# Optimization experiments

Measured on AMD Instinct MI355X. Metric: run time of the kernel, lower is better.

The kernel has to match this reference:

```python
import jax, jax.numpy as jnp
import numpy as np

N, NN = 16384, 10          # n_messages, max neighbors
IN, H = 135, 256           # input feature size, hidden size
HEADS, DPH = 4, 256 // 4   # attention heads, dim per head
DEPTH = 5
NEG_INF = -1e18


def setup_inputs() -> dict:
    key = jax.random.key(0)
    ks = jax.random.split(key, 17)
    s = lambda k, sh: (jax.random.normal(k, sh, jnp.float32) * 0.05)
    return {
        "fmess": jax.random.normal(ks[0], (N, IN), jnp.float32),
        "bgraph": jax.random.randint(ks[1], (N, NN), 0, N),
        "Wq": s(ks[2], (H, IN)), "bq": s(ks[3], (H,)),
        "Wk": s(ks[4], (H, H)), "bk": s(ks[5], (H,)),
        "Wv": s(ks[6], (H, H)), "bv": s(ks[7], (H,)),
        "alpha": s(ks[8], (1, 1, HEADS, 2 * DPH)),
        "abias": s(ks[9], (1, 1, HEADS)),
        "Wz": s(ks[10], (H, IN + H)), "bz": s(ks[11], (H,)),
        "Wr": s(ks[12], (H, IN)),
        "Ur": s(ks[13], (H, H)), "bur": s(ks[14], (H,)),
        "Wh": s(ks[15], (H, IN + H)), "bh": s(ks[16], (H,)),
    }


def reference(fmess, bgraph, Wq, bq, Wk, bk, Wv, bv, alpha, abias,
              Wz, bz, Wr, Ur, bur, Wh, bh):
    n = fmess.shape[0]
    # q depends only on fmess -> compute once (identical math to per-step recompute)
    q = (fmess @ Wq.T + bq).reshape(n, 1, HEADS, DPH)
    node_mask = jnp.ones((n, 1), jnp.float32).at[0, 0].set(0.0)

    def step(h, _):
        h_nei = h[bgraph]                                   # [n, nn, H] gather
        k = (h_nei @ Wk.T + bk).reshape(n, NN, HEADS, DPH)
        v = (h_nei @ Wv.T + bv).reshape(n, NN, HEADS, DPH)
        qb = jnp.broadcast_to(q, (n, NN, HEADS, DPH))
        qk = jax.nn.leaky_relu(jnp.concatenate([qb, k], axis=-1))  # slope 0.01
        score = jnp.sum(qk * alpha, axis=-1) + abias        # [n, nn, heads]
        attn_mask = (jnp.sum(h_nei, axis=2) == 0)[:, :, None]
        score = jnp.where(attn_mask, NEG_INF, score)
        w = jax.nn.softmax(score, axis=1)                   # softmax over neighbors
        sum_h = jnp.einsum('nmh,nmhd->nhd', w, v).reshape(n, H)
        z = jax.nn.sigmoid(jnp.concatenate([fmess, sum_h], axis=1) @ Wz.T + bz)
        r = jax.nn.sigmoid(fmess @ Wr.T + sum_h @ Ur.T + bur)
        pre_h = jnp.tanh(jnp.concatenate([fmess, r * sum_h], axis=1) @ Wh.T + bh)
        new_h = ((1.0 - z) * sum_h + z * pre_h) * node_mask
        return new_h, None

    h0 = jnp.zeros((n, H), jnp.float32)
    h, _ = jax.lax.scan(step, h0, None, length=DEPTH)
    return h
```

## Files before the change

### kernel.cpp

```cpp
#include <hip/hip_runtime.h>
#include <hip/hip_bf16.h>
#include <math.h>

#define NMSG 16384
#define NNEI 10
#define INF_ 135
#define KPAD 160
#define HID 256
#define DPH 64
#define DEPTH 5

typedef __attribute__((ext_vector_type(8))) short short8b;
typedef __attribute__((ext_vector_type(4))) float f32x4;
typedef __hip_bfloat16 bf16;

__device__ __forceinline__ float sigmoidf_(float x){ return 1.f/(1.f+expf(-x)); }
__device__ __forceinline__ float b2f(unsigned short u){ return __uint_as_float(((unsigned)u)<<16); }

__device__ __forceinline__ void gload_lds16(const void* g, void* l){
    __builtin_amdgcn_global_load_lds(
        (const __attribute__((address_space(1))) unsigned int*)g,
        (__attribute__((address_space(3))) unsigned int*)l, 16, 0, 0);
}

template<int EPI>
__global__ __launch_bounds__(256) void mm_k(
    const bf16* __restrict__ A, const bf16* __restrict__ B, int K,
    float* __restrict__ Cf,
    bf16* __restrict__ Cb0, bf16* __restrict__ Cb1, bf16* __restrict__ Cb2,
    const bf16* __restrict__ E0, const bf16* __restrict__ E1,
    const float* __restrict__ b0, const float* __restrict__ b1,
    const bf16* __restrict__ SH, const bf16* __restrict__ ZBB,
    const float* __restrict__ AL, float* __restrict__ SKout,
    float* __restrict__ Snext)
{
    constexpr int BM=128, BN=64, BK=32;
    __shared__ __align__(16) unsigned short As[BM*BK];
    __shared__ __align__(16) unsigned short Bs[BN*BK];
    const int tid = threadIdx.x;
    const int w = tid >> 6, lane = tid & 63;
    const int bm0 = blockIdx.x * BM, bn0 = blockIdx.y * BN;
    const int rq = lane >> 2, slot = lane & 3;
    const int fr = lane & 15, fs = lane >> 4;

    f32x4 acc[2][4] = {};

    for (int k0 = 0; k0 < K; k0 += BK){
        #pragma unroll
        for (int i = 0; i < 2; ++i){
            const int r0 = i*64 + w*16;
            const int r  = r0 + rq;
            const int sw = slot ^ ((r >> 1) & 3);
            gload_lds16(A + (size_t)(bm0 + r)*K + k0 + sw*8, As + r0*BK);
        }
        {
            const int r0 = w*16;
            const int r  = r0 + rq;
            const int sw = slot ^ ((r >> 1) & 3);
            gload_lds16(B + (size_t)(bn0 + r)*K + k0 + sw*8, Bs + r0*BK);
        }
        __syncthreads();
        short8b af[2], bfr[4];
        #pragma unroll
        for (int mi = 0; mi < 2; ++mi){
            const int row = w*32 + mi*16 + fr;
            const int sw = fs ^ ((row >> 1) & 3);
            af[mi] = *(const short8b*)((const char*)As + row*64 + sw*16);
        }
        #pragma unroll
        for (int ni = 0; ni < 4; ++ni){
            const int row = ni*16 + fr;
            const int sw = fs ^ ((row >> 1) & 3);
            bfr[ni] = *(const short8b*)((const char*)Bs + row*64 + sw*16);
        }
        #pragma unroll
        for (int mi = 0; mi < 2; ++mi)
            #pragma unroll
            for (int ni = 0; ni < 4; ++ni)
                acc[mi][ni] = __builtin_amdgcn_mfma_f32_16x16x32_bf16(af[mi], bfr[ni], acc[mi][ni], 0, 0, 0);
        __syncthreads();
    }

    if constexpr (EPI == 0 || EPI == 1){
        if (blockIdx.y < 4){
            const int head = blockIdx.y;
            #pragma unroll
            for (int mi = 0; mi < 2; ++mi){
                #pragma unroll
                for (int t = 0; t < 4; ++t){
                    float p = 0.f;
                    #pragma unroll
                    for (int ni = 0; ni < 4; ++ni){
                        const int d = ni*16 + fr;
                        float x = acc[mi][ni][t] + b0[head*64 + d];
                        float lr = x > 0.f ? x : 0.01f*x;
                        p = fmaf(lr, AL[head*128 + d], p);
                    }
                    p += __shfl_xor(p,1); p += __shfl_xor(p,2);
                    p += __shfl_xor(p,4); p += __shfl_xor(p,8);
                    if (fr == 0){
                        const int m = bm0 + w*32 + mi*16 + fs*4 + t;
                        SKout[m*4 + head] = p;
                    }
                }
            }
        } else {
            bf16* dst; int cbase;
            if constexpr (EPI == 0){
                const int sel = ((int)blockIdx.y - 4) >> 2;
                dst = (sel == 0) ? Cb0 : (sel == 1) ? Cb1 : Cb2;
                cbase = (((int)blockIdx.y - 4) & 3) * 64;
            } else {
                dst = Cb0;
                cbase = ((int)blockIdx.y - 4) * 64;
            }
            #pragma unroll
            for (int mi = 0; mi < 2; ++mi)
                #pragma unroll
                for (int ni = 0; ni < 4; ++ni)
                    #pragma unroll
                    for (int t = 0; t < 4; ++t){
                        const int m = bm0 + w*32 + mi*16 + fs*4 + t;
                        const int c = cbase + ni*16 + fr;
                        dst[(size_t)m*HID + c] = __float2bfloat16(acc[mi][ni][t]);
                    }
        }
    } else if constexpr (EPI == 2){
        const bool zpath = (blockIdx.y < 4);
        const int cbase = ((int)blockIdx.y & 3) * 64;
        #pragma unroll
        for (int mi = 0; mi < 2; ++mi)
            #pragma unroll
            for (int ni = 0; ni < 4; ++ni)
                #pragma unroll
                for (int t = 0; t < 4; ++t){
                    const int m = bm0 + w*32 + mi*16 + fs*4 + t;
                    const int c = cbase + ni*16 + fr;
                    const size_t off = (size_t)m*HID + c;
                    const float v = acc[mi][ni][t];
                    if (zpath){
                        Cb0[off] = __float2bfloat16(
                            sigmoidf_(v + b2f(*(const unsigned short*)&E0[off]) + b0[c]));
                    } else {
                        float r = sigmoidf_(v + b2f(*(const unsigned short*)&E1[off]) + b1[c]);
                        Cb1[off] = __float2bfloat16(r * b2f(*(const unsigned short*)&SH[off]));
                    }
                }
    } else {
        const int cbase = (int)blockIdx.y * 64;
        #pragma unroll
        for (int mi = 0; mi < 2; ++mi){
            #pragma unroll
            for (int t = 0; t < 4; ++t){
                const int m = bm0 + w*32 + mi*16 + fs*4 + t;
                float psum = 0.f;
                #pragma unroll
                for (int ni = 0; ni < 4; ++ni){
                    const int c = cbase + ni*16 + fr;
                    const size_t off = (size_t)m*HID + c;
                    const float ph = tanhf(acc[mi][ni][t] + b2f(*(const unsigned short*)&E0[off]) + b0[c]);
                    const float z  = b2f(*(const unsigned short*)&ZBB[off]);
                    const float sh = b2f(*(const unsigned short*)&SH[off]);
                    float hn = (1.f - z)*sh + z*ph;
                    if (m == 0) hn = 0.f;
                    if (Cf)  Cf[off]  = hn;
                    if (Cb0) Cb0[off] = __float2bfloat16(hn);
                    psum += hn;
                }
                if (Snext){
                    psum += __shfl_xor(psum,1); psum += __shfl_xor(psum,2);
                    psum += __shfl_xor(psum,4); psum += __shfl_xor(psum,8);
                    if (fr == 0) atomicAdd(&Snext[m], psum);
                }
            }
        }
    }
}

struct ConvSegs {
    const float* src[10];
    bf16* dst[10];
    int srcld[10], col0[10], ncols[10], dstld[10];
    int start[10];
};
__global__ __launch_bounds__(256) void convall_k(ConvSegs cs, int total){
    int i = blockIdx.x*256 + threadIdx.x;
    if (i >= total) return;
    int s = 0;
    #pragma unroll
    for (int j = 1; j < 10; ++j) if (i >= cs.start[j]) s = j;
    const int li = i - cs.start[s];
    const int ld = cs.dstld[s];
    const int r = li / ld, c = li - r*ld;
    float v = (c < cs.ncols[s]) ? cs.src[s][(size_t)r*cs.srcld[s] + cs.col0[s] + c] : 0.f;
    cs.dst[s][li] = __float2bfloat16(v);
}

__global__ __launch_bounds__(256) void bcast_k(const float* __restrict__ bv,
                                               bf16* __restrict__ sumhb){
    const int i = blockIdx.x*256 + threadIdx.x;
    sumhb[i] = __float2bfloat16(bv[i & 255]);
}

__global__ __launch_bounds__(256) void attn_k(
    const int*   __restrict__ bgraph,
    const float* __restrict__ sq,
    const float* __restrict__ sk,
    const float* __restrict__ S,
    const float* __restrict__ abias,
    const bf16*  __restrict__ V,
    const float* __restrict__ bv,
    bf16* __restrict__ sumhb)
{
    const int gid  = blockIdx.x*256 + threadIdx.x;
    const int n    = gid >> 6;
    const int lane = gid & 63;
    const int head = lane >> 4;
    const float ab  = abias[head];
    const float sqv = sq[n*4 + head];
    int g[NNEI];
    #pragma unroll
    for (int j = 0; j < NNEI; ++j) g[j] = bgraph[n*NNEI + j];
    float sc[NNEI];
    float mx = -1e30f;
    #pragma unroll
    for (int j = 0; j < NNEI; ++j){
        float s = sqv + sk[g[j]*4 + head] + ab;
        if (S[g[j]] == 0.f) s = -1e18f;
        sc[j] = s;
        mx = fmaxf(mx, s);
    }
    float den = 0.f;
    #pragma unroll
    for (int j = 0; j < NNEI; ++j){ sc[j] = expf(sc[j] - mx); den += sc[j]; }
    const float inv = 1.f/den;
    float a0=0.f, a1=0.f, a2=0.f, a3=0.f;
    #pragma unroll
    for (int j = 0; j < NNEI; ++j){
        const float w = sc[j]*inv;
        const ushort4 vv = *reinterpret_cast<const ushort4*>(
            (const unsigned short*)V + (size_t)g[j]*HID + lane*4);
        a0 = fmaf(w, b2f(vv.x), a0);
        a1 = fmaf(w, b2f(vv.y), a1);
        a2 = fmaf(w, b2f(vv.z), a2);
        a3 = fmaf(w, b2f(vv.w), a3);
    }
    const float4 bvv = *reinterpret_cast<const float4*>(bv + lane*4);
    a0 += bvv.x; a1 += bvv.y; a2 += bvv.z; a3 += bvv.w;
    ushort4 ob;
    { bf16 t0=__float2bfloat16(a0); ob.x=*(unsigned short*)&t0; }
    { bf16 t1=__float2bfloat16(a1); ob.y=*(unsigned short*)&t1; }
    { bf16 t2=__float2bfloat16(a2); ob.z=*(unsigned short*)&t2; }
    { bf16 t3=__float2bfloat16(a3); ob.w=*(unsigned short*)&t3; }
    *reinterpret_cast<ushort4*>((unsigned short*)sumhb + (size_t)n*HID + lane*4) = ob;
}

extern "C" void kernel_launch(void* const* d_in, const int* in_sizes, int n_in,
                              void* d_out, int out_size, void* d_ws, size_t ws_size,
                              hipStream_t stream) {
    const float* fmess = (const float*)d_in[0];
    const int*   bgraph= (const int*  )d_in[1];
    const float* Wq    = (const float*)d_in[2];
    const float* bq    = (const float*)d_in[3];
    const float* Wk    = (const float*)d_in[4];
    const float* bk    = (const float*)d_in[5];
    const float* Wv    = (const float*)d_in[6];
    const float* bv    = (const float*)d_in[7];
    const float* alpha = (const float*)d_in[8];
    const float* abias = (const float*)d_in[9];
    const float* Wz    = (const float*)d_in[10];
    const float* bz    = (const float*)d_in[11];
    const float* Wr    = (const float*)d_in[12];
    const float* Ur    = (const float*)d_in[13];
    const float* bur   = (const float*)d_in[14];
    const float* Wh    = (const float*)d_in[15];
    const float* bh    = (const float*)d_in[16];
    float* out = (float*)d_out;

    const size_t NH = (size_t)NMSG*HID;
    char* p = (char*)d_ws;
    auto alloc = [&](size_t bytes)->char*{ char* r = p; p += (bytes + 255) & ~(size_t)255; return r; };
    bf16* fmessb = (bf16*)alloc((size_t)NMSG*KPAD*2);
    bf16* Wcat   = (bf16*)alloc((size_t)1024*KPAD*2);
    bf16* WKV    = (bf16*)alloc((size_t)512*HID*2);
    bf16* WZR    = (bf16*)alloc((size_t)512*HID*2);
    bf16* WH     = (bf16*)alloc((size_t)256*HID*2);
    bf16* FZb    = (bf16*)alloc(NH*2);
    bf16* FRb    = (bf16*)alloc(NH*2);
    bf16* FHb    = (bf16*)alloc(NH*2);
    bf16* Vb     = (bf16*)alloc(NH*2);
    bf16* hb     = (bf16*)alloc(NH*2);
    bf16* sumhb  = (bf16*)alloc(NH*2);
    bf16* rsb    = (bf16*)alloc(NH*2);
    bf16* zbb    = (bf16*)alloc(NH*2);
    float* S_all = (float*)alloc(5*(size_t)NMSG*4);
    float* sq    = (float*)alloc((size_t)NMSG*4*4);
    float* sk    = (float*)alloc((size_t)NMSG*4*4);

    const dim3 gb(256);
    const int rgrid = NMSG*64/256;

    {
        ConvSegs cs;
        const size_t WQK = (size_t)256*KPAD;
        const float* srcs[10] = {fmess, Wq, Wz, Wr, Wh, Wk, Wv, Wz, Ur, Wh};
        bf16* dsts[10] = {fmessb, Wcat, Wcat+WQK, Wcat+2*WQK, Wcat+3*WQK,
                          WKV, WKV+(size_t)256*HID, WZR, WZR+(size_t)256*HID, WH};
        int srclds[10] = {INF_, INF_, INF_+HID, INF_, INF_+HID, HID, HID, INF_+HID, HID, INF_+HID};
        int col0s[10]  = {0,0,0,0,0, 0,0,INF_,0,INF_};
        int ncolss[10] = {INF_,INF_,INF_,INF_,INF_, HID,HID,HID,HID,HID};
        int dstlds[10] = {KPAD,KPAD,KPAD,KPAD,KPAD, HID,HID,HID,HID,HID};
        int sizes[10]  = {NMSG*KPAD, 256*KPAD,256*KPAD,256*KPAD,256*KPAD,
                          256*HID,256*HID,256*HID,256*HID,256*HID};
        int st = 0;
        for (int j = 0; j < 10; ++j){
            cs.src[j]=srcs[j]; cs.dst[j]=dsts[j]; cs.srcld[j]=srclds[j];
            cs.col0[j]=col0s[j]; cs.ncols[j]=ncolss[j]; cs.dstld[j]=dstlds[j];
            cs.start[j]=st; st += sizes[j];
        }
        convall_k<<<(st+255)/256, gb, 0, stream>>>(cs, st);
    }
    hipMemsetAsync(S_all, 0, 5*(size_t)NMSG*4, stream);

    mm_k<0><<<dim3(NMSG/128, 16), gb, 0, stream>>>(fmessb, Wcat, KPAD,
        nullptr, FZb, FRb, FHb, nullptr, nullptr, bq, nullptr, nullptr, nullptr,
        alpha, sq, nullptr);

    bcast_k<<<NH/256, gb, 0, stream>>>(bv, sumhb);
    mm_k<2><<<dim3(NMSG/128, 8), gb, 0, stream>>>(sumhb, WZR, HID,
        nullptr, zbb, rsb, nullptr, FZb, FRb, bz, bur, sumhb, nullptr,
        nullptr, nullptr, nullptr);
    mm_k<3><<<dim3(NMSG/128, 4), gb, 0, stream>>>(rsb, WH, HID,
        nullptr, hb, nullptr, nullptr, FHb, nullptr, bh, nullptr, sumhb, zbb,
        nullptr, nullptr, S_all + 1*(size_t)NMSG);

    for (int step = 1; step < DEPTH; ++step){
        const bool last = (step == DEPTH-1);
        float* cf    = last ? out : nullptr;
        bf16*  cb    = last ? nullptr : hb;
        float* Snext = last ? nullptr : (S_all + (step+1)*(size_t)NMSG);
        mm_k<1><<<dim3(NMSG/128, 8), gb, 0, stream>>>(hb, WKV, HID,
            nullptr, Vb, nullptr, nullptr, nullptr, nullptr, bk, nullptr, nullptr, nullptr,
            alpha + DPH, sk, nullptr);
        attn_k<<<rgrid, gb, 0, stream>>>(bgraph, sq, sk, S_all + step*(size_t)NMSG,
                                         abias, Vb, bv, sumhb);
        mm_k<2><<<dim3(NMSG/128, 8), gb, 0, stream>>>(sumhb, WZR, HID,
            nullptr, zbb, rsb, nullptr, FZb, FRb, bz, bur, sumhb, nullptr,
            nullptr, nullptr, nullptr);
        mm_k<3><<<dim3(NMSG/128, 4), gb, 0, stream>>>(rsb, WH, HID,
            cf, cb, nullptr, nullptr, FHb, nullptr, bh, nullptr, sumhb, zbb,
            nullptr, nullptr, Snext);
    }
}
```

Before: 451.9 us.

## Aggregate raw h before V projection and fold Wv into gate weights

Attention now gathers and averages neighbor h directly instead of the projected V, since softmax weights sum to one. The V projection moves after aggregation, and Wv is pre-multiplied into Ur and the h-part of Wz, with the biases folded in. This removes the separate V output buffer and the z-gate GEMM pass per step. The gate, reset and update GEMMs are restructured into dual-B and dual-A MFMA kernels with 64-row tiles. The mask-all-zero case still relies on the uniform-weight equivalence, and the folded weights add extra bf16 rounding.

```diff
diff --git a/kernel.cpp b/kernel.cpp
--- a/kernel.cpp
+++ b/kernel.cpp
@@ -16,6 +16,9 @@
 
 __device__ __forceinline__ float sigmoidf_(float x){ return 1.f/(1.f+expf(-x)); }
 __device__ __forceinline__ float b2f(unsigned short u){ return __uint_as_float(((unsigned)u)<<16); }
+__device__ __forceinline__ float ldb(const bf16* p, size_t off){
+    return b2f(*((const unsigned short*)p + off));
+}
 
 __device__ __forceinline__ void gload_lds16(const void* g, void* l){
     __builtin_amdgcn_global_load_lds(
@@ -25,142 +28,152 @@
 
 template<int EPI>
 __global__ __launch_bounds__(256) void mm_k(
-    const bf16* __restrict__ A, const bf16* __restrict__ B, int K,
-    float* __restrict__ Cf,
-    bf16* __restrict__ Cb0, bf16* __restrict__ Cb1, bf16* __restrict__ Cb2,
+    const bf16* __restrict__ A1, const bf16* __restrict__ A2,
+    const bf16* __restrict__ B1, const bf16* __restrict__ B2, int K,
     const bf16* __restrict__ E0, const bf16* __restrict__ E1,
     const float* __restrict__ b0, const float* __restrict__ b1,
-    const bf16* __restrict__ SH, const bf16* __restrict__ ZBB,
-    const float* __restrict__ AL, float* __restrict__ SKout,
-    float* __restrict__ Snext)
+    const bf16* __restrict__ SH,
+    float* __restrict__ Cf, bf16* __restrict__ Cb0, bf16* __restrict__ Cb1, bf16* __restrict__ Cb2,
+    const float* __restrict__ AL, float* __restrict__ SKout, float* __restrict__ Snext)
 {
-    constexpr int BM=128, BN=64, BK=32;
-    __shared__ __align__(16) unsigned short As[BM*BK];
-    __shared__ __align__(16) unsigned short Bs[BN*BK];
+    constexpr int BM = (EPI==0) ? 128 : 64;
+    constexpr int MF = BM/64;
+    constexpr int BK = 32;
+    constexpr bool DB = (EPI>=2);
+    constexpr bool DA = (EPI==3);
+    __shared__ __align__(16) unsigned short As1[BM*BK];
+    __shared__ __align__(16) unsigned short As2[DA ? BM*BK : 8];
+    __shared__ __align__(16) unsigned short Bs1[64*BK];
+    __shared__ __align__(16) unsigned short Bs2[DB ? 64*BK : 8];
     const int tid = threadIdx.x;
     const int w = tid >> 6, lane = tid & 63;
-    const int bm0 = blockIdx.x * BM, bn0 = blockIdx.y * BN;
+    const int bm0 = blockIdx.x * BM;
+    const int bn0 = blockIdx.y * 64;
     const int rq = lane >> 2, slot = lane & 3;
     const int fr = lane & 15, fs = lane >> 4;
-
-    f32x4 acc[2][4] = {};
+    const int wrow = w * (MF*16);
+
+    f32x4 acc1[MF][4] = {};
+    f32x4 acc2[MF][4] = {};
 
     for (int k0 = 0; k0 < K; k0 += BK){
         #pragma unroll
-        for (int i = 0; i < 2; ++i){
+        for (int i = 0; i < MF; ++i){
             const int r0 = i*64 + w*16;
             const int r  = r0 + rq;
             const int sw = slot ^ ((r >> 1) & 3);
-            gload_lds16(A + (size_t)(bm0 + r)*K + k0 + sw*8, As + r0*BK);
+            gload_lds16(A1 + (size_t)(bm0 + r)*K + k0 + sw*8, As1 + r0*BK);
+            if constexpr (DA)
+                gload_lds16(A2 + (size_t)(bm0 + r)*K + k0 + sw*8, As2 + r0*BK);
         }
         {
             const int r0 = w*16;
             const int r  = r0 + rq;
             const int sw = slot ^ ((r >> 1) & 3);
-            gload_lds16(B + (size_t)(bn0 + r)*K + k0 + sw*8, Bs + r0*BK);
+            gload_lds16(B1 + (size_t)(bn0 + r)*K + k0 + sw*8, Bs1 + r0*BK);
+            if constexpr (DB)
+                gload_lds16(B2 + (size_t)(bn0 + r)*K + k0 + sw*8, Bs2 + r0*BK);
         }
         __syncthreads();
-        short8b af[2], bfr[4];
-        #pragma unroll
-        for (int mi = 0; mi < 2; ++mi){
-            const int row = w*32 + mi*16 + fr;
+        short8b af1[MF], af2[MF], bv1[4], bv2[4];
+        #pragma unroll
+        for (int mi = 0; mi < MF; ++mi){
+            const int row = wrow + mi*16 + fr;
             const int sw = fs ^ ((row >> 1) & 3);
-            af[mi] = *(const short8b*)((const char*)As + row*64 + sw*16);
+            af1[mi] = *(const short8b*)((const char*)As1 + row*64 + sw*16);
+            if constexpr (DA)
+                af2[mi] = *(const short8b*)((const char*)As2 + row*64 + sw*16);
         }
         #pragma unroll
         for (int ni = 0; ni < 4; ++ni){
             const int row = ni*16 + fr;
             const int sw = fs ^ ((row >> 1) & 3);
-            bfr[ni] = *(const short8b*)((const char*)Bs + row*64 + sw*16);
-        }
-        #pragma unroll
-        for (int mi = 0; mi < 2; ++mi)
-            #pragma unroll
-            for (int ni = 0; ni < 4; ++ni)
-                acc[mi][ni] = __builtin_amdgcn_mfma_f32_16x16x32_bf16(af[mi], bfr[ni], acc[mi][ni], 0, 0, 0);
+            bv1[ni] = *(const short8b*)((const char*)Bs1 + row*64 + sw*16);
+            if constexpr (DB)
+                bv2[ni] = *(const short8b*)((const char*)Bs2 + row*64 + sw*16);
+        }
+        #pragma unroll
+        for (int mi = 0; mi < MF; ++mi)
+            #pragma unroll
+            for (int ni = 0; ni < 4; ++ni){
+                acc1[mi][ni] = __builtin_amdgcn_mfma_f32_16x16x32_bf16(af1[mi], bv1[ni], acc1[mi][ni], 0, 0, 0);
+                if constexpr (DB)
+                    acc2[mi][ni] = __builtin_amdgcn_mfma_f32_16x16x32_bf16(
+                        DA ? af2[mi] : af1[mi], bv2[ni], acc2[mi][ni], 0, 0, 0);
+            }
         __syncthreads();
     }
 
     if constexpr (EPI == 0 || EPI == 1){
-        if (blockIdx.y < 4){
+        const bool score = (EPI == 1) || (blockIdx.y < 4);
+        if (score){
             const int head = blockIdx.y;
             #pragma unroll
-            for (int mi = 0; mi < 2; ++mi){
+            for (int mi = 0; mi < MF; ++mi){
                 #pragma unroll
                 for (int t = 0; t < 4; ++t){
                     float p = 0.f;
                     #pragma unroll
                     for (int ni = 0; ni < 4; ++ni){
                         const int d = ni*16 + fr;
-                        float x = acc[mi][ni][t] + b0[head*64 + d];
+                        float x = acc1[mi][ni][t] + b0[head*64 + d];
                         float lr = x > 0.f ? x : 0.01f*x;
                         p = fmaf(lr, AL[head*128 + d], p);
                     }
                     p += __shfl_xor(p,1); p += __shfl_xor(p,2);
                     p += __shfl_xor(p,4); p += __shfl_xor(p,8);
                     if (fr == 0){
-                        const int m = bm0 + w*32 + mi*16 + fs*4 + t;
+                        const int m = bm0 + wrow + mi*16 + fs*4 + t;
                         SKout[m*4 + head] = p;
                     }
                 }
             }
         } else {
-            bf16* dst; int cbase;
-            if constexpr (EPI == 0){
-                const int sel = ((int)blockIdx.y - 4) >> 2;
-                dst = (sel == 0) ? Cb0 : (sel == 1) ? Cb1 : Cb2;
-                cbase = (((int)blockIdx.y - 4) & 3) * 64;
-            } else {
-                dst = Cb0;
-                cbase = ((int)blockIdx.y - 4) * 64;
-            }
-            #pragma unroll
-            for (int mi = 0; mi < 2; ++mi)
+            const int sel = ((int)blockIdx.y - 4) >> 2;
+            bf16* dst = (sel == 0) ? Cb0 : (sel == 1) ? Cb1 : Cb2;
+            const int cbase = (((int)blockIdx.y - 4) & 3) * 64;
+            #pragma unroll
+            for (int mi = 0; mi < MF; ++mi)
                 #pragma unroll
                 for (int ni = 0; ni < 4; ++ni)
                     #pragma unroll
                     for (int t = 0; t < 4; ++t){
-                        const int m = bm0 + w*32 + mi*16 + fs*4 + t;
+                        const int m = bm0 + wrow + mi*16 + fs*4 + t;
                         const int c = cbase + ni*16 + fr;
-                        dst[(size_t)m*HID + c] = __float2bfloat16(acc[mi][ni][t]);
+                        dst[(size_t)m*HID + c] = __float2bfloat16(acc1[mi][ni][t]);
                     }
         }
     } else if constexpr (EPI == 2){
-        const bool zpath = (blockIdx.y < 4);
-        const int cbase = ((int)blockIdx.y & 3) * 64;
-        #pragma unroll
-        for (int mi = 0; mi < 2; ++mi)
+        const int cbase = (int)blockIdx.y * 64;
+        #pragma unroll
+        for (int mi = 0; mi < MF; ++mi)
             #pragma unroll
             for (int ni = 0; ni < 4; ++ni)
                 #pragma unroll
                 for (int t = 0; t < 4; ++t){
-                    const int m = bm0 + w*32 + mi*16 + fs*4 + t;
+                    const int m = bm0 + wrow + mi*16 + fs*4 + t;
                     const int c = cbase + ni*16 + fr;
                     const size_t off = (size_t)m*HID + c;
-                    const float v = acc[mi][ni][t];
-                    if (zpath){
-                        Cb0[off] = __float2bfloat16(
-                            sigmoidf_(v + b2f(*(const unsigned short*)&E0[off]) + b0[c]));
-                    } else {
-                        float r = sigmoidf_(v + b2f(*(const unsigned short*)&E1[off]) + b1[c]);
-                        Cb1[off] = __float2bfloat16(r * b2f(*(const unsigned short*)&SH[off]));
-                    }
+                    const float sumh = acc1[mi][ni][t] + b0[c];
+                    const float r = sigmoidf_(acc2[mi][ni][t] + ldb(E1, off) + b1[c]);
+                    Cb0[off] = __float2bfloat16(sumh);
+                    Cb1[off] = __float2bfloat16(r * sumh);
                 }
     } else {
         const int cbase = (int)blockIdx.y * 64;
         #pragma unroll
-        for (int mi = 0; mi < 2; ++mi){
+        for (int mi = 0; mi < MF; ++mi){
             #pragma unroll
             for (int t = 0; t < 4; ++t){
-                const int m = bm0 + w*32 + mi*16 + fs*4 + t;
+                const int m = bm0 + wrow + mi*16 + fs*4 + t;
                 float psum = 0.f;
                 #pragma unroll
                 for (int ni = 0; ni < 4; ++ni){
                     const int c = cbase + ni*16 + fr;
                     const size_t off = (size_t)m*HID + c;
-                    const float ph = tanhf(acc[mi][ni][t] + b2f(*(const unsigned short*)&E0[off]) + b0[c]);
-                    const float z  = b2f(*(const unsigned short*)&ZBB[off]);
-                    const float sh = b2f(*(const unsigned short*)&SH[off]);
+                    const float ph = tanhf(acc1[mi][ni][t] + ldb(E0, off) + b0[c]);
+                    const float z  = sigmoidf_(acc2[mi][ni][t] + ldb(E1, off) + b1[c]);
+                    const float sh = ldb(SH, off);
                     float hn = (1.f - z)*sh + z*ph;
                     if (m == 0) hn = 0.f;
                     if (Cf)  Cf[off]  = hn;
@@ -178,17 +191,17 @@
 }
 
 struct ConvSegs {
-    const float* src[10];
-    bf16* dst[10];
-    int srcld[10], col0[10], ncols[10], dstld[10];
-    int start[10];
+    const float* src[8];
+    bf16* dst[8];
+    int srcld[8], col0[8], ncols[8], dstld[8];
+    int start[8];
 };
 __global__ __launch_bounds__(256) void convall_k(ConvSegs cs, int total){
     int i = blockIdx.x*256 + threadIdx.x;
     if (i >= total) return;
     int s = 0;
     #pragma unroll
-    for (int j = 1; j < 10; ++j) if (i >= cs.start[j]) s = j;
+    for (int j = 1; j < 8; ++j) if (i >= cs.start[j]) s = j;
     const int li = i - cs.start[s];
     const int ld = cs.dstld[s];
     const int r = li / ld, c = li - r*ld;
@@ -196,10 +209,31 @@
     cs.dst[s][li] = __float2bfloat16(v);
 }
 
-__global__ __launch_bounds__(256) void bcast_k(const float* __restrict__ bv,
-                                               bf16* __restrict__ sumhb){
-    const int i = blockIdx.x*256 + threadIdx.x;
-    sumhb[i] = __float2bfloat16(bv[i & 255]);
+__global__ __launch_bounds__(256) void wcomb_k(
+    const float* __restrict__ Ur, const float* __restrict__ Wz,
+    const float* __restrict__ Wv, const float* __restrict__ bv,
+    const float* __restrict__ bur, const float* __restrict__ bz,
+    bf16* __restrict__ Urv, bf16* __restrict__ Wzv,
+    float* __restrict__ bur2, float* __restrict__ bz2)
+{
+    const int i = blockIdx.x, j = threadIdx.x;
+    const bool zp = (i >= 256);
+    const int r = zp ? i - 256 : i;
+    const float* Arow = zp ? (Wz + (size_t)r*(INF_+HID) + INF_) : (Ur + (size_t)r*HID);
+    float acc = 0.f;
+    for (int q = 0; q < HID; ++q)
+        acc = fmaf(Arow[q], Wv[(size_t)q*HID + j], acc);
+    (zp ? Wzv : Urv)[(size_t)r*HID + j] = __float2bfloat16(acc);
+    float part = Arow[j] * bv[j];
+    part += __shfl_xor(part,1);  part += __shfl_xor(part,2);  part += __shfl_xor(part,4);
+    part += __shfl_xor(part,8);  part += __shfl_xor(part,16); part += __shfl_xor(part,32);
+    __shared__ float red[4];
+    if ((j & 63) == 0) red[j >> 6] = part;
+    __syncthreads();
+    if (j == 0){
+        float s = red[0] + red[1] + red[2] + red[3];
+        if (zp) bz2[r] = bz[r] + s; else bur2[r] = bur[r] + s;
+    }
 }
 
 __global__ __launch_bounds__(256) void attn_k(
@@ -208,9 +242,8 @@
     const float* __restrict__ sk,
     const float* __restrict__ S,
     const float* __restrict__ abias,
-    const bf16*  __restrict__ V,
-    const float* __restrict__ bv,
-    bf16* __restrict__ sumhb)
+    const bf16*  __restrict__ H,
+    bf16* __restrict__ haggb)
 {
     const int gid  = blockIdx.x*256 + threadIdx.x;
     const int n    = gid >> 6;
@@ -239,20 +272,18 @@
     for (int j = 0; j < NNEI; ++j){
         const float w = sc[j]*inv;
         const ushort4 vv = *reinterpret_cast<const ushort4*>(
-            (const unsigned short*)V + (size_t)g[j]*HID + lane*4);
+            (const unsigned short*)H + (size_t)g[j]*HID + lane*4);
         a0 = fmaf(w, b2f(vv.x), a0);
         a1 = fmaf(w, b2f(vv.y), a1);
         a2 = fmaf(w, b2f(vv.z), a2);
         a3 = fmaf(w, b2f(vv.w), a3);
     }
-    const float4 bvv = *reinterpret_cast<const float4*>(bv + lane*4);
-    a0 += bvv.x; a1 += bvv.y; a2 += bvv.z; a3 += bvv.w;
     ushort4 ob;
     { bf16 t0=__float2bfloat16(a0); ob.x=*(unsigned short*)&t0; }
     { bf16 t1=__float2bfloat16(a1); ob.y=*(unsigned short*)&t1; }
     { bf16 t2=__float2bfloat16(a2); ob.z=*(unsigned short*)&t2; }
     { bf16 t3=__float2bfloat16(a3); ob.w=*(unsigned short*)&t3; }
-    *reinterpret_cast<ushort4*>((unsigned short*)sumhb + (size_t)n*HID + lane*4) = ob;
+    *reinterpret_cast<ushort4*>((unsigned short*)haggb + (size_t)n*HID + lane*4) = ob;
 }
 
 extern "C" void kernel_launch(void* const* d_in, const int* in_sizes, int n_in,
@@ -282,18 +313,23 @@
     auto alloc = [&](size_t bytes)->char*{ char* r = p; p += (bytes + 255) & ~(size_t)255; return r; };
     bf16* fmessb = (bf16*)alloc((size_t)NMSG*KPAD*2);
     bf16* Wcat   = (bf16*)alloc((size_t)1024*KPAD*2);
-    bf16* WKV    = (bf16*)alloc((size_t)512*HID*2);
-    bf16* WZR    = (bf16*)alloc((size_t)512*HID*2);
-    bf16* WH     = (bf16*)alloc((size_t)256*HID*2);
+    bf16* Wkb    = (bf16*)alloc((size_t)256*HID*2);
+    bf16* Wvb    = (bf16*)alloc((size_t)256*HID*2);
+    bf16* Wh2b   = (bf16*)alloc((size_t)256*HID*2);
+    bf16* Urv    = (bf16*)alloc((size_t)256*HID*2);
+    bf16* Wzv    = (bf16*)alloc((size_t)256*HID*2);
+    float* bur2  = (float*)alloc(256*4);
+    float* bz2   = (float*)alloc(256*4);
     bf16* FZb    = (bf16*)alloc(NH*2);
     bf16* FRb    = (bf16*)alloc(NH*2);
     bf16* FHb    = (bf16*)alloc(NH*2);
-    bf16* Vb     = (bf16*)alloc(NH*2);
-    bf16* hb     = (bf16*)alloc(NH*2);
     bf16* sumhb  = (bf16*)alloc(NH*2);
     bf16* rsb    = (bf16*)alloc(NH*2);
-    bf16* zbb    = (bf16*)alloc(NH*2);
-    float* S_all = (float*)alloc(5*(size_t)NMSG*4);
+    char* zreg   = alloc(NH*2 + NH*2 + 5*(size_t)NMSG*4);
+    bf16*  hb    = (bf16*)zreg;
+    bf16*  haggb = (bf16*)(zreg + NH*2);
+    float* S_all = (float*)(zreg + NH*2 + NH*2);
+    const size_t zbytes = NH*2 + NH*2 + 5*(size_t)NMSG*4;
     float* sq    = (float*)alloc((size_t)NMSG*4*4);
     float* sk    = (float*)alloc((size_t)NMSG*4*4);
 
@@ -303,52 +339,46 @@
     {
         ConvSegs cs;
         const size_t WQK = (size_t)256*KPAD;
-        const float* srcs[10] = {fmess, Wq, Wz, Wr, Wh, Wk, Wv, Wz, Ur, Wh};
-        bf16* dsts[10] = {fmessb, Wcat, Wcat+WQK, Wcat+2*WQK, Wcat+3*WQK,
-                          WKV, WKV+(size_t)256*HID, WZR, WZR+(size_t)256*HID, WH};
-        int srclds[10] = {INF_, INF_, INF_+HID, INF_, INF_+HID, HID, HID, INF_+HID, HID, INF_+HID};
-        int col0s[10]  = {0,0,0,0,0, 0,0,INF_,0,INF_};
-        int ncolss[10] = {INF_,INF_,INF_,INF_,INF_, HID,HID,HID,HID,HID};
-        int dstlds[10] = {KPAD,KPAD,KPAD,KPAD,KPAD, HID,HID,HID,HID,HID};
-        int sizes[10]  = {NMSG*KPAD, 256*KPAD,256*KPAD,256*KPAD,256*KPAD,
-                          256*HID,256*HID,256*HID,256*HID,256*HID};
+        const float* srcs[8] = {fmess, Wq, Wz, Wr, Wh, Wk, Wv, Wh};
+        bf16* dsts[8] = {fmessb, Wcat, Wcat+WQK, Wcat+2*WQK, Wcat+3*WQK, Wkb, Wvb, Wh2b};
+        int srclds[8] = {INF_, INF_, INF_+HID, INF_, INF_+HID, HID, HID, INF_+HID};
+        int col0s[8]  = {0,0,0,0,0, 0,0,INF_};
+        int ncolss[8] = {INF_,INF_,INF_,INF_,INF_, HID,HID,HID};
+        int dstlds[8] = {KPAD,KPAD,KPAD,KPAD,KPAD, HID,HID,HID};
+        int sizes[8]  = {NMSG*KPAD, 256*KPAD,256*KPAD,256*KPAD,256*KPAD,
+                         256*HID,256*HID,256*HID};
         int st = 0;
-        for (int j = 0; j < 10; ++j){
+        for (int j = 0; j < 8; ++j){
             cs.src[j]=srcs[j]; cs.dst[j]=dsts[j]; cs.srcld[j]=srclds[j];
             cs.col0[j]=col0s[j]; cs.ncols[j]=ncolss[j]; cs.dstld[j]=dstlds[j];
             cs.start[j]=st; st += sizes[j];
         }
         convall_k<<<(st+255)/256, gb, 0, stream>>>(cs, st);
     }
-    hipMemsetAsync(S_all, 0, 5*(size_t)NMSG*4, stream);
-
-    mm_k<0><<<dim3(NMSG/128, 16), gb, 0, stream>>>(fmessb, Wcat, KPAD,
-        nullptr, FZb, FRb, FHb, nullptr, nullptr, bq, nullptr, nullptr, nullptr,
-        alpha, sq, nullptr);
-
-    bcast_k<<<NH/256, gb, 0, stream>>>(bv, sumhb);
-    mm_k<2><<<dim3(NMSG/128, 8), gb, 0, stream>>>(sumhb, WZR, HID,
-        nullptr, zbb, rsb, nullptr, FZb, FRb, bz, bur, sumhb, nullptr,
-        nullptr, nullptr, nullptr);
-    mm_k<3><<<dim3(NMSG/128, 4), gb, 0, stream>>>(rsb, WH, HID,
-        nullptr, hb, nullptr, nullptr, FHb, nullptr, bh, nullptr, sumhb, zbb,
-        nullptr, nullptr, S_all + 1*(size_t)NMSG);
-
-    for (int step = 1; step < DEPTH; ++step){
+    wcomb_k<<<512, gb, 0, stream>>>(Ur, Wz, Wv, bv, bur, bz, Urv, Wzv, bur2, bz2);
+    hipMemsetAsync(zreg, 0, zbytes, stream);
+
+    mm_k<0><<<dim3(NMSG/128, 16), gb, 0, stream>>>(fmessb, nullptr, Wcat, nullptr, KPAD,
+        nullptr, nullptr, bq, nullptr, nullptr,
+        nullptr, FZb, FRb, FHb, alpha, sq, nullptr);
+
+    for (int step = 0; step < DEPTH; ++step){
         const bool last = (step == DEPTH-1);
         float* cf    = last ? out : nullptr;
         bf16*  cb    = last ? nullptr : hb;
         float* Snext = last ? nullptr : (S_all + (step+1)*(size_t)NMSG);
-        mm_k<1><<<dim3(NMSG/128, 8), gb, 0, stream>>>(hb, WKV, HID,
-            nullptr, Vb, nullptr, nullptr, nullptr, nullptr, bk, nullptr, nullptr, nullptr,
-            alpha + DPH, sk, nullptr);
-        attn_k<<<rgrid, gb, 0, stream>>>(bgraph, sq, sk, S_all + step*(size_t)NMSG,
-                                         abias, Vb, bv, sumhb);
-        mm_k<2><<<dim3(NMSG/128, 8), gb, 0, stream>>>(sumhb, WZR, HID,
-            nullptr, zbb, rsb, nullptr, FZb, FRb, bz, bur, sumhb, nullptr,
-            nullptr, nullptr, nullptr);
-        mm_k<3><<<dim3(NMSG/128, 4), gb, 0, stream>>>(rsb, WH, HID,
-            cf, cb, nullptr, nullptr, FHb, nullptr, bh, nullptr, sumhb, zbb,
-            nullptr, nullptr, Snext);
-    }
-}
+        if (step > 0){
+            mm_k<1><<<dim3(NMSG/64, 4), gb, 0, stream>>>(hb, nullptr, Wkb, nullptr, HID,
+                nullptr, nullptr, bk, nullptr, nullptr,
+                nullptr, nullptr, nullptr, nullptr, alpha + DPH, sk, nullptr);
+            attn_k<<<rgrid, gb, 0, stream>>>(bgraph, sq, sk, S_all + step*(size_t)NMSG,
+                                             abias, hb, haggb);
+        }
+        mm_k<2><<<dim3(NMSG/64, 4), gb, 0, stream>>>(haggb, nullptr, Wvb, Urv, HID,
+            nullptr, FRb, bv, bur2, nullptr,
+            nullptr, sumhb, rsb, nullptr, nullptr, nullptr, nullptr);
+        mm_k<3><<<dim3(NMSG/64, 4), gb, 0, stream>>>(rsb, haggb, Wh2b, Wzv, HID,
+            FHb, FZb, bh, bz2, sumhb,
+            cf, cb, nullptr, nullptr, nullptr, nullptr, Snext);
+    }
+}
```

New measurement: 393.6 us. -12.9%, faster.
